# Kernel optimization log

Measured on AMD Instinct MI355X. Metric: run time of the kernel, lower is better.

The kernel has to match this reference:

```python
import jax, jax.numpy as jnp
import numpy as np
import math

N_HEADS = 8
EMBED = 128
HEAD_DEPTH = EMBED // N_HEADS
CLIP = 10.0
NEG_INF = 1.0e10
SCALE = math.sqrt(HEAD_DEPTH)


def setup_inputs() -> dict:
    key = jax.random.key(0)
    ks = jax.random.split(key, 8)
    B, C, N = 32, 2, 512
    Q = jax.random.normal(ks[0], (B, C, N, EMBED), dtype=jnp.float32)
    K = jax.random.normal(ks[1], (B, C, N, EMBED), dtype=jnp.float32)
    V = jax.random.normal(ks[2], (B, C, N, EMBED), dtype=jnp.float32)
    mask = jax.random.bernoulli(ks[3], 0.15, (B, C, N, 1))  # True = masked out
    stdv_qkv = 1.0 / math.sqrt(HEAD_DEPTH)
    stdv_out = 1.0 / math.sqrt(EMBED)
    # torch nn.Linear weights: (out_features, in_features)
    Wq = jax.random.uniform(ks[4], (EMBED, EMBED), jnp.float32, -stdv_qkv, stdv_qkv)
    Wk = jax.random.uniform(ks[5], (EMBED, EMBED), jnp.float32, -stdv_qkv, stdv_qkv)
    Wv = jax.random.uniform(ks[6], (EMBED, EMBED), jnp.float32, -stdv_qkv, stdv_qkv)
    Wout = jax.random.uniform(ks[7], (EMBED, EMBED), jnp.float32, -stdv_out, stdv_out)
    return {"Q": Q, "K": K, "V": V, "mask": mask,
            "Wq": Wq, "Wk": Wk, "Wv": Wv, "Wout": Wout}


def _split_heads(T):
    # (b, c, n, E) -> (b, H, c, n, d)
    b, c, n, _ = T.shape
    return T.reshape(b, c, n, N_HEADS, HEAD_DEPTH).transpose(0, 3, 1, 2, 4)


def reference(Q, K, V, mask, Wq, Wk, Wv, Wout):
    # Linear projections (torch Linear: y = x @ W.T)
    q = _split_heads(jnp.einsum('bcne,fe->bcnf', Q, Wq))
    k = _split_heads(jnp.einsum('bcne,fe->bcnf', K, Wk))
    v = _split_heads(jnp.einsum('bcne,fe->bcnf', V, Wv))
    # logits: (b, H, c, q, k)
    logits = jnp.einsum('bhcqd,bhckd->bhcqk', q, k) / SCALE
    logits = CLIP * jnp.tanh(logits)
    # mask (b, c, n, 1) -> (b, 1, c, 1, n); True -> -1e10
    m = mask[:, None, :, :, :].swapaxes(-1, -2)
    logits = jnp.where(m, -NEG_INF, logits)
    probs = jax.nn.softmax(logits, axis=-1)
    out = jnp.einsum('bhcqk,bhckd->bhcqd', probs, v)
    # combine heads: (b, H, c, n, d) -> (b, c, n, E)
    b, h, c, n, d = out.shape
    out = out.transpose(0, 2, 3, 1, 4).reshape(b, c, n, EMBED)
    return jnp.einsum('bcne,fe->bcnf', out, Wout)
```

## Files before the change

### kernel.cpp

```cpp
#include <hip/hip_runtime.h>

typedef _Float16 half_t;
typedef _Float16 half8 __attribute__((ext_vector_type(8)));
typedef _Float16 half4 __attribute__((ext_vector_type(4)));
typedef float floatx4 __attribute__((ext_vector_type(4)));
typedef float floatx16 __attribute__((ext_vector_type(16)));

#define C1 0.72134752044448170368f
#define C2 14.4269504088896340736f
#define C3 28.8539008177792681472f

__device__ __forceinline__ floatx4 zero4() {
    floatx4 z; z[0] = z[1] = z[2] = z[3] = 0.f; return z;
}
__device__ __forceinline__ floatx16 zero16() {
    floatx16 z;
#pragma unroll
    for (int i = 0; i < 16; ++i) z[i] = 0.f;
    return z;
}

__device__ __forceinline__ float pfun(float sp, float b) {
    float u = __builtin_amdgcn_exp2f(sp);
    float r = __builtin_amdgcn_rcpf(u + 1.0f);
    return __builtin_amdgcn_exp2f(b - C3 * r);
}

__global__ __launch_bounds__(256) void k_proj(
        const float* __restrict__ Q, const float* __restrict__ K,
        const float* __restrict__ V,
        const float* __restrict__ Wq, const float* __restrict__ Wk,
        const float* __restrict__ Wv, const float* __restrict__ Wo,
        half_t* __restrict__ qw, half_t* __restrict__ kw, half_t* __restrict__ vw,
        half_t* __restrict__ Who) {
    int which = blockIdx.y;
    int tid = threadIdx.x;

    if (which == 3) {
        int bx = blockIdx.x;
        if (bx < 64) {
            int idx = bx * 256 + tid;
            Who[idx] = (half_t)Wo[idx];
        }
        return;
    }

    __shared__ half_t Wl[128 * 136];

    const float* X    = (which == 0) ? Q  : (which == 1) ? K  : V;
    const float* Wsrc = (which == 0) ? Wq : (which == 1) ? Wk : Wv;
    float scale = (which == 0) ? C1 : 1.0f;

#pragma unroll
    for (int i = 0; i < 16; ++i) {
        int gidx = i * 1024 + tid * 4;
        float4 v = *(const float4*)(Wsrc + gidx);
        int f = gidx >> 7, e = gidx & 127;
        half4 hv;
        hv[0] = (half_t)(v.x * scale); hv[1] = (half_t)(v.y * scale);
        hv[2] = (half_t)(v.z * scale); hv[3] = (half_t)(v.w * scale);
        *(half4*)(Wl + f * 136 + e) = hv;
    }
    __syncthreads();

    int w = tid >> 6, lane = tid & 63;
    int l15 = lane & 15, quad = lane >> 4;
    int tokbase = blockIdx.x * 64 + w * 16;

    floatx4 acc[8];
#pragma unroll
    for (int nt = 0; nt < 8; ++nt) acc[nt] = zero4();

#pragma unroll
    for (int ks = 0; ks < 4; ++ks) {
        const float* ap = X + (tokbase + l15) * 128 + ks * 32 + quad * 8;
        float4 a0 = *(const float4*)ap;
        float4 a1 = *(const float4*)(ap + 4);
        half8 xf;
        xf[0] = (half_t)a0.x; xf[1] = (half_t)a0.y; xf[2] = (half_t)a0.z; xf[3] = (half_t)a0.w;
        xf[4] = (half_t)a1.x; xf[5] = (half_t)a1.y; xf[6] = (half_t)a1.z; xf[7] = (half_t)a1.w;
        if (which == 2) {
#pragma unroll
            for (int nt = 0; nt < 8; ++nt) {
                half8 wf = *(const half8*)(Wl + (nt * 16 + l15) * 136 + ks * 32 + quad * 8);
                acc[nt] = __builtin_amdgcn_mfma_f32_16x16x32_f16(xf, wf, acc[nt], 0, 0, 0);
            }
        } else {
#pragma unroll
            for (int nt = 0; nt < 8; ++nt) {
                half8 wf = *(const half8*)(Wl + (nt * 16 + l15) * 136 + ks * 32 + quad * 8);
                acc[nt] = __builtin_amdgcn_mfma_f32_16x16x32_f16(wf, xf, acc[nt], 0, 0, 0);
            }
        }
    }

    if (which == 2) {
        int R0 = tokbase + quad * 4;
        int bc = R0 >> 9, n0 = R0 & 511;
#pragma unroll
        for (int nt = 0; nt < 8; ++nt) {
            half4 hv;
            hv[0] = (half_t)acc[nt][0]; hv[1] = (half_t)acc[nt][1];
            hv[2] = (half_t)acc[nt][2]; hv[3] = (half_t)acc[nt][3];
            *(half4*)(vw + ((bc * 8 + nt) * 16 + l15) * 512 + n0) = hv;
        }
    } else {
        int R = tokbase + l15;
        int bc = R >> 9, n = R & 511;
        half_t* Y = (which == 0) ? qw : kw;
#pragma unroll
        for (int nt = 0; nt < 8; ++nt) {
            half4 hv;
            hv[0] = (half_t)acc[nt][0]; hv[1] = (half_t)acc[nt][1];
            hv[2] = (half_t)acc[nt][2]; hv[3] = (half_t)acc[nt][3];
            *(half4*)(Y + ((bc * 8 + nt) * 512 + n) * 16 + quad * 4) = hv;
        }
    }
}

__global__ __launch_bounds__(512, 4) void k_attn_out(
        const half_t* __restrict__ qg, const half_t* __restrict__ kg,
        const half_t* __restrict__ vTg, const int* __restrict__ mask,
        const half_t* __restrict__ Wo, float* __restrict__ out) {
    __shared__ float bias[512];
    __shared__ half_t Pb[8][32 * 36];
    __shared__ half_t attO[32 * 136];

    int bx = blockIdx.x;
    int bc = bx >> 4, qt = bx & 15;
    int tid = threadIdx.x;
    int w = tid >> 6, lane = tid & 63;
    int h = w;
    int bch = bc * 8 + h;
    int l31 = lane & 31, hf = lane >> 5;
    int l15 = lane & 15, quad = lane >> 4;

    const half_t* qh = qg + bch * 8192;
    const half_t* kh = kg + bch * 8192;
    const half_t* vh = vTg + bch * 8192;

    bias[tid] = mask[bc * 512 + tid] ? -1.0e30f : C2;
    __syncthreads();

    int qbase = qt * 32;
    half8 qf = *(const half8*)(qh + (qbase + l31) * 16 + hf * 8);

    half8 ones;
#pragma unroll
    for (int j = 0; j < 8; ++j) ones[j] = (half_t)1.0f;

    floatx4 O[2], Os[2];
    O[0] = zero4(); O[1] = zero4();
    Os[0] = zero4(); Os[1] = zero4();
    const float4* b4 = (const float4*)bias;
    half_t* Pw = &Pb[w][0];

#pragma unroll 1
    for (int c = 0; c < 16; ++c) {
        half8 kf = *(const half8*)(kh + (c * 32 + l31) * 16 + hf * 8);
        half8 vf = *(const half8*)(vh + l15 * 512 + c * 32 + quad * 8);
        float4 bv[4];
#pragma unroll
        for (int g = 0; g < 4; ++g) bv[g] = b4[c * 8 + hf + 2 * g];

        floatx16 S = __builtin_amdgcn_mfma_f32_32x32x16_f16(kf, qf, zero16(), 0, 0, 0);
#pragma unroll
        for (int g = 0; g < 4; ++g) {
            float p0 = pfun(S[4 * g + 0], bv[g].x);
            float p1 = pfun(S[4 * g + 1], bv[g].y);
            float p2 = pfun(S[4 * g + 2], bv[g].z);
            float p3 = pfun(S[4 * g + 3], bv[g].w);
            auto t0 = __builtin_amdgcn_cvt_pkrtz(p0, p1);
            auto t1 = __builtin_amdgcn_cvt_pkrtz(p2, p3);
            half4 ph;
            ph[0] = (half_t)t0[0]; ph[1] = (half_t)t0[1];
            ph[2] = (half_t)t1[0]; ph[3] = (half_t)t1[1];
            *(half4*)(Pw + l31 * 36 + hf * 4 + g * 8) = ph;
        }
#pragma unroll
        for (int nt2 = 0; nt2 < 2; ++nt2) {
            half8 pb = *(const half8*)(Pw + (nt2 * 16 + l15) * 36 + quad * 8);
            O[nt2]  = __builtin_amdgcn_mfma_f32_16x16x32_f16(vf,   pb, O[nt2],  0, 0, 0);
            Os[nt2] = __builtin_amdgcn_mfma_f32_16x16x32_f16(ones, pb, Os[nt2], 0, 0, 0);
        }
    }

#pragma unroll
    for (int nt = 0; nt < 2; ++nt) {
        float iv = __builtin_amdgcn_rcpf(Os[nt][0]);
        int qrl = nt * 16 + l15;
        half4 ov;
        ov[0] = (half_t)(O[nt][0] * iv);
        ov[1] = (half_t)(O[nt][1] * iv);
        ov[2] = (half_t)(O[nt][2] * iv);
        ov[3] = (half_t)(O[nt][3] * iv);
        *(half4*)(attO + qrl * 136 + h * 16 + quad * 4) = ov;
    }
    __syncthreads();

    int tw = w & 1, fw = w >> 1;
    const half_t* xbase = attO + (tw * 16 + l15) * 136;
    floatx4 acc2[2];
    acc2[0] = zero4(); acc2[1] = zero4();
#pragma unroll
    for (int ks = 0; ks < 4; ++ks) {
        half8 xf = *(const half8*)(xbase + ks * 32 + quad * 8);
#pragma unroll
        for (int nt = 0; nt < 2; ++nt) {
            half8 wf = *(const half8*)(Wo + (fw * 32 + nt * 16 + l15) * 128 + ks * 32 + quad * 8);
            acc2[nt] = __builtin_amdgcn_mfma_f32_16x16x32_f16(wf, xf, acc2[nt], 0, 0, 0);
        }
    }
    int tokg = bc * 512 + qt * 32 + tw * 16 + l15;
#pragma unroll
    for (int nt = 0; nt < 2; ++nt) {
        float4 o;
        o.x = acc2[nt][0]; o.y = acc2[nt][1]; o.z = acc2[nt][2]; o.w = acc2[nt][3];
        *(float4*)(out + tokg * 128 + fw * 32 + nt * 16 + quad * 4) = o;
    }
}

extern "C" void kernel_launch(void* const* d_in, const int* in_sizes, int n_in,
                              void* d_out, int out_size, void* d_ws, size_t ws_size,
                              hipStream_t stream) {
    const float* Q    = (const float*)d_in[0];
    const float* K    = (const float*)d_in[1];
    const float* V    = (const float*)d_in[2];
    const int*   mask = (const int*)d_in[3];
    const float* Wq   = (const float*)d_in[4];
    const float* Wk   = (const float*)d_in[5];
    const float* Wv   = (const float*)d_in[6];
    const float* Wo   = (const float*)d_in[7];
    float* out = (float*)d_out;

    half_t* ws = (half_t*)d_ws;
    half_t* Who = ws + 49152;
    half_t* qw  = ws + 65536;
    half_t* kw  = qw + 4194304;
    half_t* vw  = kw + 4194304;

    k_proj<<<dim3(512, 4), 256, 0, stream>>>(Q, K, V, Wq, Wk, Wv, Wo,
                                             qw, kw, vw, Who);
    k_attn_out<<<1024, 512, 0, stream>>>(qw, kw, vw, mask, Who, out);
}
```

Measured before the change: 160.1 us.

## Compact unmasked keys/values in projection and skip masked key tiles in attention

```diff
diff --git a/kernel.cpp b/kernel.cpp
--- a/kernel.cpp
+++ b/kernel.cpp
@@ -28,7 +28,7 @@
 
 __global__ __launch_bounds__(256) void k_proj(
         const float* __restrict__ Q, const float* __restrict__ K,
-        const float* __restrict__ V,
+        const float* __restrict__ V, const int* __restrict__ mask,
         const float* __restrict__ Wq, const float* __restrict__ Wk,
         const float* __restrict__ Wv, const float* __restrict__ Wo,
         half_t* __restrict__ qw, half_t* __restrict__ kw, half_t* __restrict__ vw,
@@ -46,10 +46,24 @@
     }
 
     __shared__ half_t Wl[128 * 136];
+    __shared__ unsigned long long cwv[8];
+    __shared__ int wps[9];
 
     const float* X    = (which == 0) ? Q  : (which == 1) ? K  : V;
     const float* Wsrc = (which == 0) ? Wq : (which == 1) ? Wk : Wv;
     float scale = (which == 0) ? C1 : 1.0f;
+
+    int bxx = blockIdx.x;
+    int bc = bxx >> 3;
+    int w = tid >> 6, lane = tid & 63;
+
+    if (which != 0) {
+        int m0 = mask[bc * 512 + tid];
+        int m1 = mask[bc * 512 + 256 + tid];
+        unsigned long long b0 = __ballot(m0 == 0);
+        unsigned long long b1 = __ballot(m1 == 0);
+        if (lane == 0) { cwv[w] = b0; cwv[4 + w] = b1; }
+    }
 
 #pragma unroll
     for (int i = 0; i < 16; ++i) {
@@ -63,9 +77,38 @@
     }
     __syncthreads();
 
-    int w = tid >> 6, lane = tid & 63;
+    if (which != 0 && tid == 0) {
+        int acc = 0;
+#pragma unroll
+        for (int j = 0; j < 8; ++j) { wps[j] = acc; acc += __popcll(cwv[j]); }
+        wps[8] = acc;
+    }
+    if (which != 0) __syncthreads();
+
+    if (which != 0 && (bxx & 7) == 7) {
+        int cnt = wps[8];
+        int pad = (((cnt + 31) >> 5) << 5) - cnt;
+        if (which == 1) {
+            half8 z8;
+#pragma unroll
+            for (int j = 0; j < 8; ++j) z8[j] = (half_t)0.f;
+            for (int u = tid; u < 8 * 64; u += 256) {
+                int nt = u >> 6, rem = u & 63;
+                int p = rem >> 1, off = (rem & 1) * 8;
+                if (p < pad)
+                    *(half8*)(kw + (((bc * 8 + nt) * 512) + cnt + p) * 16 + off) = z8;
+            }
+        } else {
+            for (int u = tid; u < 128 * 32; u += 256) {
+                int r = u >> 5, p = u & 31;
+                if (p < pad)
+                    vw[(bc * 128 + r) * 512 + cnt + p] = (half_t)0.f;
+            }
+        }
+    }
+
     int l15 = lane & 15, quad = lane >> 4;
-    int tokbase = blockIdx.x * 64 + w * 16;
+    int tokbase = bxx * 64 + w * 16;
 
     floatx4 acc[8];
 #pragma unroll
@@ -95,25 +138,46 @@
     }
 
     if (which == 2) {
-        int R0 = tokbase + quad * 4;
-        int bc = R0 >> 9, n0 = R0 & 511;
+        int n0 = (tokbase & 511) + quad * 4;
+        int s_r[4]; bool keep_r[4];
+#pragma unroll
+        for (int r = 0; r < 4; ++r) {
+            int n = n0 + r;
+            unsigned long long cword = cwv[n >> 6];
+            keep_r[r] = (cword >> (n & 63)) & 1ull;
+            s_r[r] = wps[n >> 6] + __popcll(cword & ((1ull << (n & 63)) - 1ull));
+        }
+#pragma unroll
+        for (int nt = 0; nt < 8; ++nt) {
+#pragma unroll
+            for (int r = 0; r < 4; ++r) {
+                if (keep_r[r])
+                    vw[((bc * 8 + nt) * 16 + l15) * 512 + s_r[r]] = (half_t)acc[nt][r];
+            }
+        }
+    } else if (which == 1) {
+        int n = (tokbase & 511) + l15;
+        unsigned long long cword = cwv[n >> 6];
+        bool keep = (cword >> (n & 63)) & 1ull;
+        int s = wps[n >> 6] + __popcll(cword & ((1ull << (n & 63)) - 1ull));
+        if (keep) {
+#pragma unroll
+            for (int nt = 0; nt < 8; ++nt) {
+                half4 hv;
+                hv[0] = (half_t)acc[nt][0]; hv[1] = (half_t)acc[nt][1];
+                hv[2] = (half_t)acc[nt][2]; hv[3] = (half_t)acc[nt][3];
+                *(half4*)(kw + ((bc * 8 + nt) * 512 + s) * 16 + quad * 4) = hv;
+            }
+        }
+    } else {
+        int R = tokbase + l15;
+        int n = R & 511;
 #pragma unroll
         for (int nt = 0; nt < 8; ++nt) {
             half4 hv;
             hv[0] = (half_t)acc[nt][0]; hv[1] = (half_t)acc[nt][1];
             hv[2] = (half_t)acc[nt][2]; hv[3] = (half_t)acc[nt][3];
-            *(half4*)(vw + ((bc * 8 + nt) * 16 + l15) * 512 + n0) = hv;
-        }
-    } else {
-        int R = tokbase + l15;
-        int bc = R >> 9, n = R & 511;
-        half_t* Y = (which == 0) ? qw : kw;
-#pragma unroll
-        for (int nt = 0; nt < 8; ++nt) {
-            half4 hv;
-            hv[0] = (half_t)acc[nt][0]; hv[1] = (half_t)acc[nt][1];
-            hv[2] = (half_t)acc[nt][2]; hv[3] = (half_t)acc[nt][3];
-            *(half4*)(Y + ((bc * 8 + nt) * 512 + n) * 16 + quad * 4) = hv;
+            *(half4*)(qw + ((bc * 8 + nt) * 512 + n) * 16 + quad * 4) = hv;
         }
     }
 }
@@ -123,6 +187,7 @@
         const half_t* __restrict__ vTg, const int* __restrict__ mask,
         const half_t* __restrict__ Wo, float* __restrict__ out) {
     __shared__ float bias[512];
+    __shared__ int redc[8];
     __shared__ half_t Pb[8][32 * 36];
     __shared__ half_t attO[32 * 136];
 
@@ -139,8 +204,14 @@
     const half_t* kh = kg + bch * 8192;
     const half_t* vh = vTg + bch * 8192;
 
-    bias[tid] = mask[bc * 512 + tid] ? -1.0e30f : C2;
+    unsigned long long bal = __ballot(mask[bc * 512 + tid] == 0);
+    if (lane == 0) redc[w] = __popcll(bal);
     __syncthreads();
+    int cnt = redc[0] + redc[1] + redc[2] + redc[3]
+            + redc[4] + redc[5] + redc[6] + redc[7];
+    bias[tid] = (tid < cnt) ? C2 : -1.0e30f;
+    __syncthreads();
+    int NT = (cnt + 31) >> 5;
 
     int qbase = qt * 32;
     half8 qf = *(const half8*)(qh + (qbase + l31) * 16 + hf * 8);
@@ -156,7 +227,7 @@
     half_t* Pw = &Pb[w][0];
 
 #pragma unroll 1
-    for (int c = 0; c < 16; ++c) {
+    for (int c = 0; c < NT; ++c) {
         half8 kf = *(const half8*)(kh + (c * 32 + l31) * 16 + hf * 8);
         half8 vf = *(const half8*)(vh + l15 * 512 + c * 32 + quad * 8);
         float4 bv[4];
@@ -239,7 +310,7 @@
     half_t* kw  = qw + 4194304;
     half_t* vw  = kw + 4194304;
 
-    k_proj<<<dim3(512, 4), 256, 0, stream>>>(Q, K, V, Wq, Wk, Wv, Wo,
+    k_proj<<<dim3(512, 4), 256, 0, stream>>>(Q, K, V, mask, Wq, Wk, Wv, Wo,
                                              qw, kw, vw, Who);
     k_attn_out<<<1024, 512, 0, stream>>>(qw, kw, vw, mask, Who, out);
 }
```

Result: no change. 161.5 us (+0.8%).
